# Performance work log

Hardware: AMD Instinct MI355X
Metric: run time of the kernel (lower is better)

## Reference

```python
import jax, jax.numpy as jnp
import numpy as np

B = 64          # num_graphs per batch
ADJ = 1000      # adj_shape (nodes per graph)
N = B * ADJ     # total nodes
E = 1 << 20     # edges
M = 32000       # selected (batch, node) pairs
D_IN = 128
D_OUT = 128


def setup_inputs() -> dict:
    key = jax.random.key(0)
    ks = jax.random.split(key, 12)
    inp = {
        "x0": jax.random.normal(ks[0], (N, D_IN), jnp.float32),
        "x1": jax.random.normal(ks[1], (N, D_IN), jnp.float32),
        "edge_index": jax.random.randint(ks[2], (2, E), 0, N, jnp.int64),
        "b_idx0": jax.random.randint(ks[3], (M,), 0, B, jnp.int64),
        "n_idx0": jax.random.randint(ks[4], (M,), 0, ADJ, jnp.int64),
        "b_idx1": jax.random.randint(ks[5], (M,), 0, B, jnp.int64),
        "n_idx1": jax.random.randint(ks[6], (M,), 0, ADJ, jnp.int64),
        "W1": jax.random.normal(ks[7], (D_IN, D_IN), jnp.float32) / np.sqrt(D_IN),
        "b1": jnp.zeros((D_IN,), jnp.float32),
        "W2": jax.random.normal(ks[8], (D_IN, D_IN), jnp.float32) / np.sqrt(D_IN),
        "b2": jnp.zeros((D_IN,), jnp.float32),
        "Wl": jax.random.normal(ks[9], (D_IN, D_OUT), jnp.float32) / np.sqrt(D_IN),
        "bl": jnp.zeros((D_OUT,), jnp.float32),
        "Wfi": jax.random.normal(ks[10], (D_IN, D_OUT), jnp.float32) / np.sqrt(D_IN),
        "bfi": jnp.zeros((D_OUT,), jnp.float32),
    }
    return inp


def _gnn_layer(h, edge_index, W, b):
    # GCN-style message passing: gather source features, scatter-sum to dst,
    # then linear project.  h: [N, d]
    msgs = h[edge_index[0]]                                    # [E, d] gather
    agg = jax.ops.segment_sum(msgs, edge_index[1], num_segments=N)  # [N, d]
    return agg @ W + b


def reference(x0, x1, edge_index, b_idx0, n_idx0, b_idx1, n_idx1,
              W1, b1, W2, b2, Wl, bl, Wfi, bfi):
    # branch i == 0: raw features -> 2D gather -> fc_in
    d0 = x0.reshape(B, ADJ, -1)[b_idx0, n_idx0]                # [M, D_IN]
    d0 = d0 @ Wfi + bfi                                        # [M, D_OUT]

    # branch i == 1 (observ=True): gnn1 -> gnn2 -> 2D gather -> linear
    # (dropout omitted for deterministic reference; p=0.2 at train time)
    h = _gnn_layer(x1, edge_index, W1, b1)
    h = _gnn_layer(h, edge_index, W2, b2)
    d1 = h.reshape(B, ADJ, -1)[b_idx1, n_idx1]                 # [M, D_IN]
    d1 = d1 @ Wl + bl                                          # [M, D_OUT]

    return jnp.stack([d0, d1])                                 # [2, M, D_OUT]
```

## Files before the change

kernel.cpp:

```cpp
#include <hip/hip_runtime.h>
#include <hip/hip_bf16.h>


#define B_    64
#define ADJ_  1000
#define N_    64000
#define E_    (1 << 20)
#define M_    32000
#define DV    128
#define CAP   64
#define RANGES 8
#define RSPAN  (N_ / RANGES)
#define CHUNKS 512
#define EPB    (E_ / CHUNKS)

typedef __attribute__((ext_vector_type(8))) short short8v;
typedef __attribute__((ext_vector_type(4))) float float4v;
typedef __attribute__((ext_vector_type(4))) int   int4v;

__device__ __forceinline__ float u2f(unsigned int u) {
  union { unsigned int i; float f; } x; x.i = u; return x.f;
}
__device__ __forceinline__ unsigned short f2bf(float f) {
  union { float f; unsigned int i; } x; x.f = f;
  unsigned int r = x.i + 0x7fffu + ((x.i >> 16) & 1u);
  return (unsigned short)(r >> 16);
}
__device__ __forceinline__ unsigned int pack_bf2(float a, float b) {
  __hip_bfloat162 h = __float22bfloat162_rn(float2{a, b});
  union { __hip_bfloat162 h; unsigned int u; } c; c.h = h;
  return c.u;
}

__global__ __launch_bounds__(256)
void prep(const float* __restrict__ W1, const float* __restrict__ W2,
          const float* __restrict__ Wl, const float* __restrict__ Wfi,
          unsigned short* __restrict__ wf, int* __restrict__ counts) {
  int t = blockIdx.x * 256 + threadIdx.x;
  if (t < 4 * 16384) {
    int mtx = t >> 14, g = t & 16383;
    const float* W = mtx == 0 ? W1 : mtx == 1 ? W2 : mtx == 2 ? Wl : Wfi;
    int k = g >> 7, n = g & 127;
    int addr = ((((n >> 4) * 4 + (k >> 5)) * 64 + ((k >> 3) & 3) * 16 + (n & 15)) << 3)
             + (k & 7);
    wf[mtx * 16384 + addr] = f2bf(W[g]);
  } else {
    int c = t - 65536;
    if (c < N_) counts[c] = 0;
  }
}

__device__ __forceinline__ void fill_part(const int* __restrict__ ei,
                                          int* __restrict__ counts,
                                          unsigned short* __restrict__ bucket,
                                          int c, int r) {
  const int* srcA = ei;
  const int* dstA = ei + E_;
  int lo = r * RSPAN;
  int t4 = c * EPB + (int)threadIdx.x * 4;
  int4v d0 = __builtin_nontemporal_load((const int4v*)(dstA + t4));
  int4v s0 = __builtin_nontemporal_load((const int4v*)(srcA + t4));
  int4v d1 = __builtin_nontemporal_load((const int4v*)(dstA + t4 + 1024));
  int4v s1 = __builtin_nontemporal_load((const int4v*)(srcA + t4 + 1024));
#define PROC(D, S) do {                                                \
    if ((unsigned)((D) - lo) < (unsigned)RSPAN) {                      \
      int pos = atomicAdd(&counts[(D)], 1);                            \
      if (pos < CAP) bucket[(size_t)(D) * CAP + pos] = (unsigned short)(S); \
    } } while (0)
  PROC(d0.x, s0.x); PROC(d0.y, s0.y); PROC(d0.z, s0.z); PROC(d0.w, s0.w);
  PROC(d1.x, s1.x); PROC(d1.y, s1.y); PROC(d1.z, s1.z); PROC(d1.w, s1.w);
#undef PROC
}

template<bool GATHER, bool OUTBF16, bool HASBIAS>
__device__ __forceinline__ void gemm_g(const float* __restrict__ in,
                                       const unsigned short* __restrict__ wf,
                                       const float* __restrict__ bias,
                                       void* __restrict__ out_, int tile,
                                       const int* __restrict__ bidx,
                                       const int* __restrict__ nidx) {
  int lane = threadIdx.x & 63, wv = threadIdx.x >> 6;
  int m = lane & 15, q = lane >> 4;
  int rbase = tile * 64 + wv * 16;
  int r = rbase + m;
  size_t ir = GATHER ? (size_t)bidx[r] * ADJ_ + nidx[r] : (size_t)r;
  const float* arow = in + ir * DV;

  short8v af[4];
#pragma unroll
  for (int kc = 0; kc < 4; kc++) {
    const float4* p = (const float4*)(arow + kc * 32 + q * 8);
    float4 f0 = p[0], f1 = p[1];
    union { short8v s; unsigned int u[4]; } t;
    t.u[0] = pack_bf2(f0.x, f0.y);
    t.u[1] = pack_bf2(f0.z, f0.w);
    t.u[2] = pack_bf2(f1.x, f1.y);
    t.u[3] = pack_bf2(f1.z, f1.w);
    af[kc] = t.s;
  }

  float4v acc[8];
#pragma unroll
  for (int nb = 0; nb < 8; nb++) acc[nb] = (float4v){0.f, 0.f, 0.f, 0.f};
#pragma unroll
  for (int nb = 0; nb < 8; nb++)
#pragma unroll
    for (int kc = 0; kc < 4; kc++) {
      short8v bf = *(const short8v*)(wf + (((nb * 4 + kc) * 64 + lane) << 3));
      acc[nb] = __builtin_amdgcn_mfma_f32_16x16x32_bf16(af[kc], bf, acc[nb], 0, 0, 0);
    }

#pragma unroll
  for (int nb = 0; nb < 8; nb++) {
    float bvn = HASBIAS ? bias[nb * 16 + m] : 0.f;
    int col = nb * 16 + m;
#pragma unroll
    for (int i = 0; i < 4; i++) {
      int row = rbase + q * 4 + i;
      float v = acc[nb][i] + bvn;
      if (OUTBF16) ((unsigned short*)out_)[(size_t)row * DV + col] = f2bf(v);
      else         ((float*)out_)[(size_t)row * DV + col] = v;
    }
  }
}

__global__ __launch_bounds__(256)
void k1(const int* __restrict__ ei, int* __restrict__ counts,
        unsigned short* __restrict__ bucket,
        const float* __restrict__ x1, const unsigned short* __restrict__ wf1,
        unsigned int* __restrict__ t1,
        const float* __restrict__ x0, const unsigned short* __restrict__ wff,
        const float* __restrict__ bfi, float* __restrict__ out0,
        const int* __restrict__ b0, const int* __restrict__ n0i) {
  int g = blockIdx.x >> 4, rem = blockIdx.x & 15;
  if (rem < 8) { fill_part(ei, counts, bucket, g, rem); return; }
  int o = g * 8 + rem - 8;
  if (o < 1000)
    gemm_g<false, true, false>(x1, wf1, nullptr, t1, o, nullptr, nullptr);
  else if (o < 1500)
    gemm_g<true, false, true>(x0, wff, bfi, out0, o - 1000, b0, n0i);
}

template<bool SEL, bool OUTBF16, bool BIAS2>
__global__ __launch_bounds__(256)
void agg_gemm(const unsigned int* __restrict__ x,
              const int* __restrict__ counts,
              const unsigned short* __restrict__ bucket,
              const float* __restrict__ bias1,
              const unsigned short* __restrict__ wf,
              const float* __restrict__ bias2, void* __restrict__ out_,
              const int* __restrict__ bidx, const int* __restrict__ nidx) {
  __shared__ unsigned int As[64 * 68];
  int tid = threadIdx.x, lane = tid & 63, wv = tid >> 6;
  int tile = blockIdx.x;
  float2 bv = ((const float2*)bias1)[lane];

  for (int i = 0; i < 16; i++) {
    int rl = wv * 16 + i;
    int grow = tile * 64 + rl;
    int node = SEL ? (bidx[grow] * ADJ_ + nidx[grow]) : grow;
    int cnt = counts[node]; cnt = min(cnt, CAP);
    int mysrc = (int)bucket[(size_t)node * CAP + lane];
    float accx = bv.x, accy = bv.y;
    int d = 0;
    for (; d + 4 <= cnt; d += 4) {
      int s0 = __shfl(mysrc, d, 64);
      int s1 = __shfl(mysrc, d + 1, 64);
      int s2 = __shfl(mysrc, d + 2, 64);
      int s3 = __shfl(mysrc, d + 3, 64);
      unsigned int u0 = x[(size_t)s0 * 64 + lane];
      unsigned int u1 = x[(size_t)s1 * 64 + lane];
      unsigned int u2 = x[(size_t)s2 * 64 + lane];
      unsigned int u3 = x[(size_t)s3 * 64 + lane];
      accx += (u2f(u0 << 16) + u2f(u1 << 16)) + (u2f(u2 << 16) + u2f(u3 << 16));
      accy += (u2f(u0 & 0xffff0000u) + u2f(u1 & 0xffff0000u))
            + (u2f(u2 & 0xffff0000u) + u2f(u3 & 0xffff0000u));
    }
    for (; d < cnt; d++) {
      int s = __shfl(mysrc, d, 64);
      unsigned int u = x[(size_t)s * 64 + lane];
      accx += u2f(u << 16);
      accy += u2f(u & 0xffff0000u);
    }
    As[rl * 68 + lane] = pack_bf2(accx, accy);
  }
  __syncthreads();

  int m = lane & 15, q = lane >> 4;
  const unsigned short* As16 = (const unsigned short*)As;
  short8v af[4];
#pragma unroll
  for (int kc = 0; kc < 4; kc++)
    af[kc] = *(const short8v*)(As16 + (wv * 16 + m) * 136 + kc * 32 + q * 8);

  float4v acc[8];
#pragma unroll
  for (int nb = 0; nb < 8; nb++) acc[nb] = (float4v){0.f, 0.f, 0.f, 0.f};
#pragma unroll
  for (int nb = 0; nb < 8; nb++)
#pragma unroll
    for (int kc = 0; kc < 4; kc++) {
      short8v bf = *(const short8v*)(wf + (((nb * 4 + kc) * 64 + lane) << 3));
      acc[nb] = __builtin_amdgcn_mfma_f32_16x16x32_bf16(af[kc], bf, acc[nb], 0, 0, 0);
    }

#pragma unroll
  for (int nb = 0; nb < 8; nb++) {
    float bvn = BIAS2 ? bias2[nb * 16 + m] : 0.f;
    int col = nb * 16 + m;
#pragma unroll
    for (int i = 0; i < 4; i++) {
      int row = tile * 64 + wv * 16 + q * 4 + i;
      float v = acc[nb][i] + bvn;
      if (OUTBF16) ((unsigned short*)out_)[(size_t)row * DV + col] = f2bf(v);
      else         ((float*)out_)[(size_t)row * DV + col] = v;
    }
  }
}

extern "C" void kernel_launch(void* const* d_in, const int* in_sizes, int n_in,
                              void* d_out, int out_size, void* d_ws, size_t ws_size,
                              hipStream_t stream) {
  const float* x0  = (const float*)d_in[0];
  const float* x1  = (const float*)d_in[1];
  const int*   ei  = (const int*)  d_in[2];
  const int*   b0  = (const int*)  d_in[3];
  const int*   n0i = (const int*)  d_in[4];
  const int*   b1  = (const int*)  d_in[5];
  const int*   n1i = (const int*)  d_in[6];
  const float* W1  = (const float*)d_in[7];
  const float* bb1 = (const float*)d_in[8];
  const float* W2  = (const float*)d_in[9];
  const float* bb2 = (const float*)d_in[10];
  const float* Wl  = (const float*)d_in[11];
  const float* bl  = (const float*)d_in[12];
  const float* Wfi = (const float*)d_in[13];
  const float* bfi = (const float*)d_in[14];
  float* out = (float*)d_out;

  unsigned int*   t1     = (unsigned int*)d_ws;
  unsigned int*   t2     = t1 + (size_t)N_ * 64;
  int*            counts = (int*)(t2 + (size_t)N_ * 64);
  unsigned short* bucket = (unsigned short*)(counts + N_);
  unsigned short* wf     = bucket + (size_t)N_ * CAP;
  unsigned short* wf1 = wf, *wf2 = wf + 16384, *wfl = wf + 32768, *wff = wf + 49152;

  prep<<<(4 * 16384 + N_ + 255) / 256, 256, 0, stream>>>(W1, W2, Wl, Wfi, wf, counts);

  k1<<<CHUNKS * 16, 256, 0, stream>>>(ei, counts, bucket, x1, wf1, t1,
                                      x0, wff, bfi, out, b0, n0i);

  agg_gemm<false, true, false><<<N_ / 64, 256, 0, stream>>>(
      t1, counts, bucket, bb1, wf2, nullptr, t2, nullptr, nullptr);

  agg_gemm<true, false, true><<<M_ / 64, 256, 0, stream>>>(
      t2, counts, bucket, bb2, wfl, bl, out + (size_t)M_ * DV, b1, n1i);
}
```

Measured before the change: 305.8 us.

## Split fused aggregate+GEMM into separate wave-per-node aggregate and GEMM kernels

Replaces the fused agg_gemm kernel, where each wave aggregated 16 nodes serially before an MFMA GEMM, with a separate aggregate kernel that gives each node its own wave and issues 16 gathers in flight. A bf16-input GEMM kernel then projects the result. The aim is more memory-level parallelism and occupancy in the latency-bound gather. The cost is two extra launches and a bf16 intermediate round trip through global memory. It also drops the nontemporal hints on the edge-index loads.

```diff
diff --git a/kernel.cpp b/kernel.cpp
--- a/kernel.cpp
+++ b/kernel.cpp
@@ -16,7 +16,6 @@
 
 typedef __attribute__((ext_vector_type(8))) short short8v;
 typedef __attribute__((ext_vector_type(4))) float float4v;
-typedef __attribute__((ext_vector_type(4))) int   int4v;
 
 __device__ __forceinline__ float u2f(unsigned int u) {
   union { unsigned int i; float f; } x; x.i = u; return x.f;
@@ -58,10 +57,10 @@
   const int* dstA = ei + E_;
   int lo = r * RSPAN;
   int t4 = c * EPB + (int)threadIdx.x * 4;
-  int4v d0 = __builtin_nontemporal_load((const int4v*)(dstA + t4));
-  int4v s0 = __builtin_nontemporal_load((const int4v*)(srcA + t4));
-  int4v d1 = __builtin_nontemporal_load((const int4v*)(dstA + t4 + 1024));
-  int4v s1 = __builtin_nontemporal_load((const int4v*)(srcA + t4 + 1024));
+  int4 d0 = *(const int4*)(dstA + t4);
+  int4 s0 = *(const int4*)(srcA + t4);
+  int4 d1 = *(const int4*)(dstA + t4 + 1024);
+  int4 s1 = *(const int4*)(srcA + t4 + 1024);
 #define PROC(D, S) do {                                                \
     if ((unsigned)((D) - lo) < (unsigned)RSPAN) {                      \
       int pos = atomicAdd(&counts[(D)], 1);                            \
@@ -72,8 +71,8 @@
 #undef PROC
 }
 
-template<bool GATHER, bool OUTBF16, bool HASBIAS>
-__device__ __forceinline__ void gemm_g(const float* __restrict__ in,
+template<bool GATHER, bool ABF16, bool OUTBF16, bool HASBIAS>
+__device__ __forceinline__ void gemm_g(const void* __restrict__ in,
                                        const unsigned short* __restrict__ wf,
                                        const float* __restrict__ bias,
                                        void* __restrict__ out_, int tile,
@@ -84,19 +83,26 @@
   int rbase = tile * 64 + wv * 16;
   int r = rbase + m;
   size_t ir = GATHER ? (size_t)bidx[r] * ADJ_ + nidx[r] : (size_t)r;
-  const float* arow = in + ir * DV;
 
   short8v af[4];
-#pragma unroll
-  for (int kc = 0; kc < 4; kc++) {
-    const float4* p = (const float4*)(arow + kc * 32 + q * 8);
-    float4 f0 = p[0], f1 = p[1];
-    union { short8v s; unsigned int u[4]; } t;
-    t.u[0] = pack_bf2(f0.x, f0.y);
-    t.u[1] = pack_bf2(f0.z, f0.w);
-    t.u[2] = pack_bf2(f1.x, f1.y);
-    t.u[3] = pack_bf2(f1.z, f1.w);
-    af[kc] = t.s;
+  if (ABF16) {
+    const unsigned short* arow = (const unsigned short*)in + ir * DV;
+#pragma unroll
+    for (int kc = 0; kc < 4; kc++)
+      af[kc] = *(const short8v*)(arow + kc * 32 + q * 8);
+  } else {
+    const float* arow = (const float*)in + ir * DV;
+#pragma unroll
+    for (int kc = 0; kc < 4; kc++) {
+      const float4* p = (const float4*)(arow + kc * 32 + q * 8);
+      float4 f0 = p[0], f1 = p[1];
+      union { short8v s; unsigned int u[4]; } t;
+      t.u[0] = pack_bf2(f0.x, f0.y);
+      t.u[1] = pack_bf2(f0.z, f0.w);
+      t.u[2] = pack_bf2(f1.x, f1.y);
+      t.u[3] = pack_bf2(f1.z, f1.w);
+      af[kc] = t.s;
+    }
   }
 
   float4v acc[8];
@@ -136,86 +142,50 @@
   if (rem < 8) { fill_part(ei, counts, bucket, g, rem); return; }
   int o = g * 8 + rem - 8;
   if (o < 1000)
-    gemm_g<false, true, false>(x1, wf1, nullptr, t1, o, nullptr, nullptr);
+    gemm_g<false, false, true, false>(x1, wf1, nullptr, t1, o, nullptr, nullptr);
   else if (o < 1500)
-    gemm_g<true, false, true>(x0, wff, bfi, out0, o - 1000, b0, n0i);
-}
-
-template<bool SEL, bool OUTBF16, bool BIAS2>
-__global__ __launch_bounds__(256)
-void agg_gemm(const unsigned int* __restrict__ x,
-              const int* __restrict__ counts,
-              const unsigned short* __restrict__ bucket,
-              const float* __restrict__ bias1,
-              const unsigned short* __restrict__ wf,
-              const float* __restrict__ bias2, void* __restrict__ out_,
-              const int* __restrict__ bidx, const int* __restrict__ nidx) {
-  __shared__ unsigned int As[64 * 68];
-  int tid = threadIdx.x, lane = tid & 63, wv = tid >> 6;
-  int tile = blockIdx.x;
-  float2 bv = ((const float2*)bias1)[lane];
-
-  for (int i = 0; i < 16; i++) {
-    int rl = wv * 16 + i;
-    int grow = tile * 64 + rl;
-    int node = SEL ? (bidx[grow] * ADJ_ + nidx[grow]) : grow;
-    int cnt = counts[node]; cnt = min(cnt, CAP);
-    int mysrc = (int)bucket[(size_t)node * CAP + lane];
-    float accx = bv.x, accy = bv.y;
-    int d = 0;
-    for (; d + 4 <= cnt; d += 4) {
-      int s0 = __shfl(mysrc, d, 64);
-      int s1 = __shfl(mysrc, d + 1, 64);
-      int s2 = __shfl(mysrc, d + 2, 64);
-      int s3 = __shfl(mysrc, d + 3, 64);
-      unsigned int u0 = x[(size_t)s0 * 64 + lane];
-      unsigned int u1 = x[(size_t)s1 * 64 + lane];
-      unsigned int u2 = x[(size_t)s2 * 64 + lane];
-      unsigned int u3 = x[(size_t)s3 * 64 + lane];
-      accx += (u2f(u0 << 16) + u2f(u1 << 16)) + (u2f(u2 << 16) + u2f(u3 << 16));
-      accy += (u2f(u0 & 0xffff0000u) + u2f(u1 & 0xffff0000u))
-            + (u2f(u2 & 0xffff0000u) + u2f(u3 & 0xffff0000u));
-    }
-    for (; d < cnt; d++) {
-      int s = __shfl(mysrc, d, 64);
-      unsigned int u = x[(size_t)s * 64 + lane];
-      accx += u2f(u << 16);
-      accy += u2f(u & 0xffff0000u);
-    }
-    As[rl * 68 + lane] = pack_bf2(accx, accy);
-  }
-  __syncthreads();
-
-  int m = lane & 15, q = lane >> 4;
-  const unsigned short* As16 = (const unsigned short*)As;
-  short8v af[4];
-#pragma unroll
-  for (int kc = 0; kc < 4; kc++)
-    af[kc] = *(const short8v*)(As16 + (wv * 16 + m) * 136 + kc * 32 + q * 8);
-
-  float4v acc[8];
-#pragma unroll
-  for (int nb = 0; nb < 8; nb++) acc[nb] = (float4v){0.f, 0.f, 0.f, 0.f};
-#pragma unroll
-  for (int nb = 0; nb < 8; nb++)
-#pragma unroll
-    for (int kc = 0; kc < 4; kc++) {
-      short8v bf = *(const short8v*)(wf + (((nb * 4 + kc) * 64 + lane) << 3));
-      acc[nb] = __builtin_amdgcn_mfma_f32_16x16x32_bf16(af[kc], bf, acc[nb], 0, 0, 0);
-    }
-
-#pragma unroll
-  for (int nb = 0; nb < 8; nb++) {
-    float bvn = BIAS2 ? bias2[nb * 16 + m] : 0.f;
-    int col = nb * 16 + m;
-#pragma unroll
-    for (int i = 0; i < 4; i++) {
-      int row = tile * 64 + wv * 16 + q * 4 + i;
-      float v = acc[nb][i] + bvn;
-      if (OUTBF16) ((unsigned short*)out_)[(size_t)row * DV + col] = f2bf(v);
-      else         ((float*)out_)[(size_t)row * DV + col] = v;
-    }
-  }
+    gemm_g<true, false, false, true>(x0, wff, bfi, out0, o - 1000, b0, n0i);
+}
+
+template<bool GATHER, bool ABF16, bool OUTBF16, bool HASBIAS>
+__global__ __launch_bounds__(256)
+void gemm_k(const void* __restrict__ in, const unsigned short* __restrict__ wf,
+            const float* __restrict__ bias, void* __restrict__ out_,
+            const int* __restrict__ bidx, const int* __restrict__ nidx) {
+  gemm_g<GATHER, ABF16, OUTBF16, HASBIAS>(in, wf, bias, out_, blockIdx.x, bidx, nidx);
+}
+
+template<bool SEL>
+__global__ __launch_bounds__(256)
+void aggregate_k(const unsigned int* __restrict__ x,
+                 const int* __restrict__ counts,
+                 const unsigned short* __restrict__ bucket,
+                 const float* __restrict__ bias, unsigned int* __restrict__ out,
+                 const int* __restrict__ bidx, const int* __restrict__ nidx) {
+  int w    = (blockIdx.x * 256 + threadIdx.x) >> 6;
+  int lane = threadIdx.x & 63;
+  int node = SEL ? (bidx[w] * ADJ_ + nidx[w]) : w;
+  int cnt = counts[node]; cnt = min(cnt, CAP);
+  int mysrc = (int)bucket[(size_t)node * CAP + lane];
+  float2 bv = ((const float2*)bias)[lane];
+  float accx = bv.x, accy = bv.y;
+
+  for (int d = 0; d < cnt; d += 16) {
+    unsigned int u[16];
+#pragma unroll
+    for (int j = 0; j < 16; j++) {
+      int jj = min(d + j, cnt - 1);
+      int s = __shfl(mysrc, jj, 64);
+      u[j] = x[(size_t)s * 64 + lane];
+    }
+#pragma unroll
+    for (int j = 0; j < 16; j++) {
+      unsigned int uv = (d + j < cnt) ? u[j] : 0u;
+      accx += u2f(uv << 16);
+      accy += u2f(uv & 0xffff0000u);
+    }
+  }
+  out[(size_t)w * 64 + lane] = pack_bf2(accx, accy);
 }
 
 extern "C" void kernel_launch(void* const* d_in, const int* in_sizes, int n_in,
@@ -238,21 +208,25 @@
   const float* bfi = (const float*)d_in[14];
   float* out = (float*)d_out;
 
-  unsigned int*   t1     = (unsigned int*)d_ws;
-  unsigned int*   t2     = t1 + (size_t)N_ * 64;
-  int*            counts = (int*)(t2 + (size_t)N_ * 64);
+  unsigned int*   bufA   = (unsigned int*)d_ws;
+  unsigned int*   bufB   = bufA + (size_t)N_ * 64;
+  int*            counts = (int*)(bufB + (size_t)N_ * 64);
   unsigned short* bucket = (unsigned short*)(counts + N_);
   unsigned short* wf     = bucket + (size_t)N_ * CAP;
   unsigned short* wf1 = wf, *wf2 = wf + 16384, *wfl = wf + 32768, *wff = wf + 49152;
 
   prep<<<(4 * 16384 + N_ + 255) / 256, 256, 0, stream>>>(W1, W2, Wl, Wfi, wf, counts);
 
-  k1<<<CHUNKS * 16, 256, 0, stream>>>(ei, counts, bucket, x1, wf1, t1,
+  k1<<<CHUNKS * 16, 256, 0, stream>>>(ei, counts, bucket, x1, wf1, bufA,
                                       x0, wff, bfi, out, b0, n0i);
 
-  agg_gemm<false, true, false><<<N_ / 64, 256, 0, stream>>>(
-      t1, counts, bucket, bb1, wf2, nullptr, t2, nullptr, nullptr);
-
-  agg_gemm<true, false, true><<<M_ / 64, 256, 0, stream>>>(
-      t2, counts, bucket, bb2, wfl, bl, out + (size_t)M_ * DV, b1, n1i);
-}
+  aggregate_k<false><<<N_ / 4, 256, 0, stream>>>(bufA, counts, bucket, bb1,
+                                                 bufB, nullptr, nullptr);
+  gemm_k<false, true, true, false><<<N_ / 64, 256, 0, stream>>>(bufB, wf2, nullptr,
+                                                                bufA, nullptr, nullptr);
+  aggregate_k<true><<<M_ / 4, 256, 0, stream>>>(bufA, counts, bucket, bb2,
+                                                bufB, b1, n1i);
+  gemm_k<false, true, false, true><<<M_ / 64, 256, 0, stream>>>(bufB, wfl, bl,
+                                                                out + (size_t)M_ * DV,
+                                                                nullptr, nullptr);
+}
```

Result: faster. 273.3 us (-10.6%).
